# Performance work log

Measured on AMD Instinct MI355X. Metric: run time of the kernel, lower is better.

The kernel has to match this reference:

```python
import jax, jax.numpy as jnp
import numpy as np

N, Q, K, H, C = 32, 1, 2048, 16, 64
E = H * C  # 1024
N_ACT = 2


def setup_inputs() -> dict:
    key = jax.random.key(0)
    ks = jax.random.split(key, 8)
    q = jax.random.normal(ks[0], (N, Q, E), dtype=jnp.float32)
    k = jax.random.normal(ks[1], (N, K, H, C), dtype=jnp.float32)
    v = jax.random.normal(ks[2], (N, K, H, C), dtype=jnp.float32)
    m = jnp.ones((N, K), dtype=bool)
    s_in = 1.0 / np.sqrt(E)
    W_in = jax.random.uniform(ks[3], (N_ACT * E, E), jnp.float32, -s_in, s_in)
    b_in = jax.random.uniform(ks[4], (N_ACT * E,), jnp.float32, -s_in, s_in)
    W_out = jax.random.uniform(ks[5], (E, E), jnp.float32, -s_in, s_in)
    b_out = jax.random.uniform(ks[6], (E,), jnp.float32, -s_in, s_in)
    return {"q": q, "k": k, "v": v, "m": m, "W_in": W_in, "b_in": b_in,
            "W_out": W_out, "b_out": b_out}


def reference(q, k, v, m, W_in, b_in, W_out, b_out):
    norm = jnp.sqrt(jnp.asarray(C, q.dtype))
    # in_proj then split into per-branch queries: [N,Q,H,C] each
    qp = (q @ W_in.T + b_in).reshape(N, Q, H, N_ACT * C)
    q_smax, q_coda = qp[..., :C], qp[..., C:]
    mexp = m[:, None, :, None]  # [N,1,K,1]

    # branch 1: masked softmax over keys
    aff_s = jnp.einsum('nqhc,nkhc->nqkh', q_smax / norm, k)
    aff_s = jnp.where(mexp, aff_s, -jnp.inf)
    aff_s = jax.nn.softmax(aff_s, axis=-2)

    # branch 2: compositional de-attention (tanh affinity * sigmoid gate)
    aff_c = jnp.tanh(jnp.einsum('nqhc,nkhc->nqkh', q_coda / norm, k))
    gate = -jnp.abs(q_coda[:, :, None] - k[:, None]).sum(-1) / norm  # [N,Q,K,H]
    gate = 2.0 * jax.nn.sigmoid(gate) * mexp.astype(q.dtype)
    aff_c = aff_c * gate

    aff = (aff_s + aff_c) / N_ACT
    mix = jnp.einsum('nqkh,nkhc->nqhc', aff, v)  # [N,Q,H,C]
    return mix.reshape(N, Q, E) @ W_out.T + b_out
```

## Files before the change

kernel.cpp:

```cpp
#include <hip/hip_runtime.h>

#define NB 32
#define KK 2048
#define HH 16
#define CC 64
#define EE 1024
#define RIN 2048
#define HC 1024
#define CHUNK 32
#define NCH (KK / CHUNK)

__device__ __forceinline__ float dot4(const float4 a, const float4 b) {
    return fmaf(a.x, b.x, fmaf(a.y, b.y, fmaf(a.z, b.z, a.w * b.w)));
}

__device__ __forceinline__ float rcp_fast(float x) {
    return __builtin_amdgcn_rcpf(x);
}

__device__ __forceinline__ float tanh_fast(float x) {
    x = fminf(fmaxf(x, -15.0f), 15.0f);
    float t = __expf(2.0f * x);
    return (t - 1.0f) * rcp_fast(t + 1.0f);
}

__device__ __forceinline__ float gate_fn(float a) {
    return 2.0f * rcp_fast(1.0f + __expf(a));
}

__device__ __forceinline__ void gload_lds16(const float* g, float* l) {
    __builtin_amdgcn_global_load_lds(
        (const __attribute__((address_space(1))) void*)g,
        (__attribute__((address_space(3))) void*)l,
        16, 0, 2);
}

__global__ __launch_bounds__(256) void gemv_batched(
        const float* __restrict__ X,
        const float* __restrict__ W,
        const float* __restrict__ b,
        float* __restrict__ Y,
        int ystride) {
    const int tid  = threadIdx.x;
    const int lane = tid & 63;
    const int w    = tid >> 6;
    const int r    = blockIdx.x * 4 + w;
    const float* Wr = W + (size_t)r * EE;

    float acc[NB];
#pragma unroll
    for (int n = 0; n < NB; ++n) acc[n] = 0.0f;

#pragma unroll
    for (int ch = 0; ch < EE; ch += 256) {
        const float4 wv = *(const float4*)(Wr + ch + lane * 4);
#pragma unroll
        for (int n = 0; n < NB; ++n) {
            const float4 xv = *(const float4*)(X + n * EE + ch + lane * 4);
            acc[n] = fmaf(wv.x, xv.x, acc[n]);
            acc[n] = fmaf(wv.y, xv.y, acc[n]);
            acc[n] = fmaf(wv.z, xv.z, acc[n]);
            acc[n] = fmaf(wv.w, xv.w, acc[n]);
        }
    }
#pragma unroll
    for (int n = 0; n < NB; ++n) {
#pragma unroll
        for (int m = 32; m >= 1; m >>= 1)
            acc[n] += __shfl_xor(acc[n], m);
    }
    if (lane == 0) {
        const float bb = b[r];
#pragma unroll
        for (int n = 0; n < NB; ++n)
            Y[n * ystride + r] = acc[n] + bb;
    }
}

#define ABLK 512
__global__ __launch_bounds__(ABLK, 4) void attn_kernel(
        const float* __restrict__ Kp,
        const float* __restrict__ Vp,
        const float* __restrict__ qp,
        float* __restrict__ mix) {
    __shared__ float bufK[4][CHUNK][CC];
    __shared__ float bufV[4][CHUNK][CC];
    __shared__ float A_part[8][CC];
    __shared__ float C_part[8][CC];
    __shared__ float redm[8];
    __shared__ float reds[8];

    const int tid  = threadIdx.x;
    const int lane = tid & 63;
    const int w    = tid >> 6;
    const int rw   = lane >> 4;
    const int c16  = lane & 15;
    const int n    = blockIdx.x >> 4;
    const int h    = blockIdx.x & 15;

    const float* qrow = qp + n * RIN + h * (2 * CC) + c16 * 4;
    const float4 qs = *(const float4*)(qrow);
    const float4 qc = *(const float4*)(qrow + CC);

    const size_t base = (size_t)n * KK * HC + h * CC;
    const float* kb = Kp + base;
    const float* vb = Vp + base;

    const size_t g_lane_off = (size_t)(lane >> 4) * HC + (lane & 15) * 4;

#define STAGE(c, slot)                                                          \
    {                                                                           \
        const size_t ro_ = (size_t)((c) * CHUNK + w * 4) * HC + g_lane_off;     \
        gload_lds16(kb + ro_, &bufK[(slot)][w * 4][0]);                         \
        gload_lds16(vb + ro_, &bufV[(slot)][w * 4][0]);                         \
    }

#define WAITV(c)                                                                \
    {                                                                           \
        if ((c) <= NCH - 3)      asm volatile("s_waitcnt vmcnt(4)" ::: "memory"); \
        else if ((c) == NCH - 2) asm volatile("s_waitcnt vmcnt(2)" ::: "memory"); \
        else                     asm volatile("s_waitcnt vmcnt(0)" ::: "memory"); \
        __builtin_amdgcn_sched_barrier(0);                                      \
    }

#define BAR_LGKM()                                                              \
    {                                                                           \
        asm volatile("s_waitcnt lgkmcnt(0)" ::: "memory");                      \
        __builtin_amdgcn_s_barrier();                                           \
        __builtin_amdgcn_sched_barrier(0);                                      \
    }

#define COMP(c, slot)                                                           \
    {                                                                           \
        const int r_ = w * 4 + rw;                                              \
        const float4 kv = *(const float4*)&bufK[(slot)][r_][c16 * 4];           \
        const float4 vv = *(const float4*)&bufV[(slot)][r_][c16 * 4];           \
        float ds = dot4(qs, kv);                                                \
        float dc = dot4(qc, kv);                                                \
        float ga = fabsf(qc.x - kv.x) + fabsf(qc.y - kv.y)                      \
                 + fabsf(qc.z - kv.z) + fabsf(qc.w - kv.w);                     \
        ds += __shfl_xor(ds, 1); ds += __shfl_xor(ds, 2);                       \
        ds += __shfl_xor(ds, 4); ds += __shfl_xor(ds, 8);                       \
        dc += __shfl_xor(dc, 1); dc += __shfl_xor(dc, 2);                       \
        dc += __shfl_xor(dc, 4); dc += __shfl_xor(dc, 8);                       \
        ga += __shfl_xor(ga, 1); ga += __shfl_xor(ga, 2);                       \
        ga += __shfl_xor(ga, 4); ga += __shfl_xor(ga, 8);                       \
        const float s_   = ds * 0.125f;                                         \
        const float cval = tanh_fast(dc * 0.125f) * gate_fn(ga * 0.125f);       \
        const float mn = fmaxf(m_run, s_);                                      \
        const float f  = __expf(m_run - mn);                                    \
        const float e  = __expf(s_ - mn);                                       \
        m_run = mn;                                                             \
        S_run = fmaf(S_run, f, e);                                              \
        A.x = fmaf(A.x, f, e * vv.x); A.y = fmaf(A.y, f, e * vv.y);             \
        A.z = fmaf(A.z, f, e * vv.z); A.w = fmaf(A.w, f, e * vv.w);             \
        Cv.x = fmaf(cval, vv.x, Cv.x); Cv.y = fmaf(cval, vv.y, Cv.y);           \
        Cv.z = fmaf(cval, vv.z, Cv.z); Cv.w = fmaf(cval, vv.w, Cv.w);           \
    }

    float m_run = -1e30f, S_run = 0.0f;
    float4 A  = make_float4(0.f, 0.f, 0.f, 0.f);
    float4 Cv = make_float4(0.f, 0.f, 0.f, 0.f);

    STAGE(0, 0); STAGE(1, 1); STAGE(2, 2);
    for (int cc = 0; cc < NCH; cc += 4) {
        WAITV(cc + 0);
        STAGE(cc + 3, 3);
        COMP(cc + 0, 0);
        WAITV(cc + 1);
        if (cc + 4 < NCH) STAGE(cc + 4, 0);
        COMP(cc + 1, 1);
        WAITV(cc + 2);
        if (cc + 5 < NCH) STAGE(cc + 5, 1);
        COMP(cc + 2, 2);
        WAITV(cc + 3);
        if (cc + 6 < NCH) STAGE(cc + 6, 2);
        COMP(cc + 3, 3);
    }

    float mw = m_run;
    mw = fmaxf(mw, __shfl_xor(mw, 16));
    mw = fmaxf(mw, __shfl_xor(mw, 32));
    if (lane == 0) redm[w] = mw;
    BAR_LGKM();
    float M = redm[0];
#pragma unroll
    for (int ww = 1; ww < 8; ++ww) M = fmaxf(M, redm[ww]);

    const float f = __expf(m_run - M);
    S_run *= f;
    A.x *= f; A.y *= f; A.z *= f; A.w *= f;
#pragma unroll
    for (int m = 16; m <= 32; m <<= 1) {
        S_run += __shfl_xor(S_run, m);
        A.x += __shfl_xor(A.x, m); A.y += __shfl_xor(A.y, m);
        A.z += __shfl_xor(A.z, m); A.w += __shfl_xor(A.w, m);
        Cv.x += __shfl_xor(Cv.x, m); Cv.y += __shfl_xor(Cv.y, m);
        Cv.z += __shfl_xor(Cv.z, m); Cv.w += __shfl_xor(Cv.w, m);
    }
    if (lane < 16) {
        *(float4*)&A_part[w][c16 * 4] = A;
        *(float4*)&C_part[w][c16 * 4] = Cv;
    }
    if (lane == 0) reds[w] = S_run;
    BAR_LGKM();
    if (tid < CC) {
        float St = 0.0f;
#pragma unroll
        for (int ww = 0; ww < 8; ++ww) St += reds[ww];
        float a = 0.0f, c_ = 0.0f;
#pragma unroll
        for (int ww = 0; ww < 8; ++ww) {
            a  += A_part[ww][tid];
            c_ += C_part[ww][tid];
        }
        mix[n * EE + h * CC + tid] = a * (0.5f / St) + 0.5f * c_;
    }
#undef STAGE
#undef WAITV
#undef BAR_LGKM
#undef COMP
}

extern "C" void kernel_launch(void* const* d_in, const int* in_sizes, int n_in,
                              void* d_out, int out_size, void* d_ws, size_t ws_size,
                              hipStream_t stream) {
    const float* q     = (const float*)d_in[0];
    const float* k     = (const float*)d_in[1];
    const float* v     = (const float*)d_in[2];
    const float* W_in  = (const float*)d_in[4];
    const float* b_in  = (const float*)d_in[5];
    const float* W_out = (const float*)d_in[6];
    const float* b_out = (const float*)d_in[7];
    float* out = (float*)d_out;

    float* qp  = (float*)d_ws;
    float* mix = qp + NB * RIN;

    gemv_batched<<<RIN / 4, 256, 0, stream>>>(q, W_in, b_in, qp, RIN);
    attn_kernel<<<NB * HH, ABLK, 0, stream>>>(k, v, qp, mix);
    gemv_batched<<<EE / 4, 256, 0, stream>>>(mix, W_out, b_out, out, EE);
}
```

Measured before the change: 137.8 us.

## Split attention over key segments with head-pair blocks and a merge kernel

```diff
diff --git a/kernel.cpp b/kernel.cpp
--- a/kernel.cpp
+++ b/kernel.cpp
@@ -7,11 +7,15 @@
 #define EE 1024
 #define RIN 2048
 #define HC 1024
-#define CHUNK 32
-#define NCH (KK / CHUNK)
-
-__device__ __forceinline__ float dot4(const float4 a, const float4 b) {
-    return fmaf(a.x, b.x, fmaf(a.y, b.y, fmaf(a.z, b.z, a.w * b.w)));
+#define NSEG 4
+#define SROWS (KK / NSEG)
+#define CHUNK 16
+#define NCH (SROWS / CHUNK)
+
+typedef float f32x4 __attribute__((ext_vector_type(4)));
+
+__device__ __forceinline__ float dot4f(const f32x4 a, const f32x4 b) {
+    return fmaf(a[0], b[0], fmaf(a[1], b[1], fmaf(a[2], b[2], a[3] * b[3])));
 }
 
 __device__ __forceinline__ float rcp_fast(float x) {
@@ -77,48 +81,58 @@
     }
 }
 
-#define ABLK 512
-__global__ __launch_bounds__(ABLK, 4) void attn_kernel(
+__global__ __launch_bounds__(256, 4) void attn_kernel(
         const float* __restrict__ Kp,
         const float* __restrict__ Vp,
         const float* __restrict__ qp,
-        float* __restrict__ mix) {
-    __shared__ float bufK[4][CHUNK][CC];
-    __shared__ float bufV[4][CHUNK][CC];
-    __shared__ float A_part[8][CC];
-    __shared__ float C_part[8][CC];
-    __shared__ float redm[8];
-    __shared__ float reds[8];
+        float* __restrict__ pm,
+        float* __restrict__ pS,
+        float* __restrict__ pA,
+        float* __restrict__ pC) {
+    __shared__ float bufK[4][CHUNK][128];
+    __shared__ float bufV[4][CHUNK][128];
+    __shared__ float A_part[4][128];
+    __shared__ float C_part[4][128];
+    __shared__ float redm[4][2];
+    __shared__ float reds[4][2];
 
     const int tid  = threadIdx.x;
     const int lane = tid & 63;
     const int w    = tid >> 6;
     const int rw   = lane >> 4;
     const int c16  = lane & 15;
-    const int n    = blockIdx.x >> 4;
-    const int h    = blockIdx.x & 15;
-
-    const float* qrow = qp + n * RIN + h * (2 * CC) + c16 * 4;
-    const float4 qs = *(const float4*)(qrow);
-    const float4 qc = *(const float4*)(qrow + CC);
-
-    const size_t base = (size_t)n * KK * HC + h * CC;
-    const float* kb = Kp + base;
-    const float* vb = Vp + base;
-
-    const size_t g_lane_off = (size_t)(lane >> 4) * HC + (lane & 15) * 4;
+    const int hb   = c16 >> 3;
+    const int b    = blockIdx.x;
+    const int n    = b >> 5;
+    const int hp   = (b >> 2) & 7;
+    const int s    = b & 3;
+
+    const int qh = hp * 2 + hb;
+    const float* qrow = qp + n * RIN + qh * (2 * CC) + (c16 & 7) * 8;
+    const f32x4 qsa = *(const f32x4*)(qrow);
+    const f32x4 qsb = *(const f32x4*)(qrow + 4);
+    const f32x4 qca = *(const f32x4*)(qrow + CC);
+    const f32x4 qcb = *(const f32x4*)(qrow + CC + 4);
+
+    const size_t gbase = ((size_t)n * KK + s * SROWS) * HC + hp * 128;
+    const float* kb0 = Kp + gbase;
+    const float* vb0 = Vp + gbase;
+
+    const size_t g_lane_off = (size_t)(lane >> 5) * HC + (lane & 31) * 4;
 
 #define STAGE(c, slot)                                                          \
     {                                                                           \
         const size_t ro_ = (size_t)((c) * CHUNK + w * 4) * HC + g_lane_off;     \
-        gload_lds16(kb + ro_, &bufK[(slot)][w * 4][0]);                         \
-        gload_lds16(vb + ro_, &bufV[(slot)][w * 4][0]);                         \
+        gload_lds16(kb0 + ro_,                  &bufK[(slot)][w * 4][0]);       \
+        gload_lds16(kb0 + ro_ + 2 * (size_t)HC, &bufK[(slot)][w * 4 + 2][0]);   \
+        gload_lds16(vb0 + ro_,                  &bufV[(slot)][w * 4][0]);       \
+        gload_lds16(vb0 + ro_ + 2 * (size_t)HC, &bufV[(slot)][w * 4 + 2][0]);   \
     }
 
 #define WAITV(c)                                                                \
     {                                                                           \
-        if ((c) <= NCH - 3)      asm volatile("s_waitcnt vmcnt(4)" ::: "memory"); \
-        else if ((c) == NCH - 2) asm volatile("s_waitcnt vmcnt(2)" ::: "memory"); \
+        if ((c) <= NCH - 3)      asm volatile("s_waitcnt vmcnt(8)" ::: "memory"); \
+        else if ((c) == NCH - 2) asm volatile("s_waitcnt vmcnt(4)" ::: "memory"); \
         else                     asm volatile("s_waitcnt vmcnt(0)" ::: "memory"); \
         __builtin_amdgcn_sched_barrier(0);                                      \
     }
@@ -130,96 +144,121 @@
         __builtin_amdgcn_sched_barrier(0);                                      \
     }
 
-#define COMP(c, slot)                                                           \
+#define COMP(slot)                                                              \
     {                                                                           \
         const int r_ = w * 4 + rw;                                              \
-        const float4 kv = *(const float4*)&bufK[(slot)][r_][c16 * 4];           \
-        const float4 vv = *(const float4*)&bufV[(slot)][r_][c16 * 4];           \
-        float ds = dot4(qs, kv);                                                \
-        float dc = dot4(qc, kv);                                                \
-        float ga = fabsf(qc.x - kv.x) + fabsf(qc.y - kv.y)                      \
-                 + fabsf(qc.z - kv.z) + fabsf(qc.w - kv.w);                     \
-        ds += __shfl_xor(ds, 1); ds += __shfl_xor(ds, 2);                       \
-        ds += __shfl_xor(ds, 4); ds += __shfl_xor(ds, 8);                       \
-        dc += __shfl_xor(dc, 1); dc += __shfl_xor(dc, 2);                       \
-        dc += __shfl_xor(dc, 4); dc += __shfl_xor(dc, 8);                       \
-        ga += __shfl_xor(ga, 1); ga += __shfl_xor(ga, 2);                       \
-        ga += __shfl_xor(ga, 4); ga += __shfl_xor(ga, 8);                       \
+        const f32x4 k0 = *(const f32x4*)&bufK[(slot)][r_][c16 * 8];             \
+        const f32x4 k1 = *(const f32x4*)&bufK[(slot)][r_][c16 * 8 + 4];         \
+        const f32x4 v0 = *(const f32x4*)&bufV[(slot)][r_][c16 * 8];             \
+        const f32x4 v1 = *(const f32x4*)&bufV[(slot)][r_][c16 * 8 + 4];         \
+        float ds = dot4f(qsa, k0) + dot4f(qsb, k1);                             \
+        float dc = dot4f(qca, k0) + dot4f(qcb, k1);                             \
+        float ga = fabsf(qca[0] - k0[0]) + fabsf(qca[1] - k0[1])                \
+                 + fabsf(qca[2] - k0[2]) + fabsf(qca[3] - k0[3])                \
+                 + fabsf(qcb[0] - k1[0]) + fabsf(qcb[1] - k1[1])                \
+                 + fabsf(qcb[2] - k1[2]) + fabsf(qcb[3] - k1[3]);               \
+        ds += __shfl_xor(ds, 1); ds += __shfl_xor(ds, 2); ds += __shfl_xor(ds, 4); \
+        dc += __shfl_xor(dc, 1); dc += __shfl_xor(dc, 2); dc += __shfl_xor(dc, 4); \
+        ga += __shfl_xor(ga, 1); ga += __shfl_xor(ga, 2); ga += __shfl_xor(ga, 4); \
         const float s_   = ds * 0.125f;                                         \
         const float cval = tanh_fast(dc * 0.125f) * gate_fn(ga * 0.125f);       \
         const float mn = fmaxf(m_run, s_);                                      \
-        const float f  = __expf(m_run - mn);                                    \
+        const float fr = __expf(m_run - mn);                                    \
         const float e  = __expf(s_ - mn);                                       \
         m_run = mn;                                                             \
-        S_run = fmaf(S_run, f, e);                                              \
-        A.x = fmaf(A.x, f, e * vv.x); A.y = fmaf(A.y, f, e * vv.y);             \
-        A.z = fmaf(A.z, f, e * vv.z); A.w = fmaf(A.w, f, e * vv.w);             \
-        Cv.x = fmaf(cval, vv.x, Cv.x); Cv.y = fmaf(cval, vv.y, Cv.y);           \
-        Cv.z = fmaf(cval, vv.z, Cv.z); Cv.w = fmaf(cval, vv.w, Cv.w);           \
+        S_run = fmaf(S_run, fr, e);                                             \
+        A0 = A0 * fr + v0 * e;  A1 = A1 * fr + v1 * e;                          \
+        Cv0 = Cv0 + v0 * cval;  Cv1 = Cv1 + v1 * cval;                          \
     }
 
     float m_run = -1e30f, S_run = 0.0f;
-    float4 A  = make_float4(0.f, 0.f, 0.f, 0.f);
-    float4 Cv = make_float4(0.f, 0.f, 0.f, 0.f);
+    f32x4 A0 = {0.f, 0.f, 0.f, 0.f}, A1 = A0, Cv0 = A0, Cv1 = A0;
 
     STAGE(0, 0); STAGE(1, 1); STAGE(2, 2);
     for (int cc = 0; cc < NCH; cc += 4) {
         WAITV(cc + 0);
         STAGE(cc + 3, 3);
-        COMP(cc + 0, 0);
+        COMP(0);
         WAITV(cc + 1);
         if (cc + 4 < NCH) STAGE(cc + 4, 0);
-        COMP(cc + 1, 1);
+        COMP(1);
         WAITV(cc + 2);
         if (cc + 5 < NCH) STAGE(cc + 5, 1);
-        COMP(cc + 2, 2);
+        COMP(2);
         WAITV(cc + 3);
         if (cc + 6 < NCH) STAGE(cc + 6, 2);
-        COMP(cc + 3, 3);
-    }
-
-    float mw = m_run;
-    mw = fmaxf(mw, __shfl_xor(mw, 16));
+        COMP(3);
+    }
+
+    float mw = fmaxf(m_run, __shfl_xor(m_run, 16));
     mw = fmaxf(mw, __shfl_xor(mw, 32));
-    if (lane == 0) redm[w] = mw;
+    if (rw == 0 && (c16 & 7) == 0) redm[w][hb] = mw;
     BAR_LGKM();
-    float M = redm[0];
-#pragma unroll
-    for (int ww = 1; ww < 8; ++ww) M = fmaxf(M, redm[ww]);
-
-    const float f = __expf(m_run - M);
-    S_run *= f;
-    A.x *= f; A.y *= f; A.z *= f; A.w *= f;
+    const float M = fmaxf(fmaxf(redm[0][hb], redm[1][hb]),
+                          fmaxf(redm[2][hb], redm[3][hb]));
+
+    const float fr = __expf(m_run - M);
+    S_run *= fr;
+    A0 = A0 * fr; A1 = A1 * fr;
+    S_run += __shfl_xor(S_run, 16); S_run += __shfl_xor(S_run, 32);
 #pragma unroll
     for (int m = 16; m <= 32; m <<= 1) {
-        S_run += __shfl_xor(S_run, m);
-        A.x += __shfl_xor(A.x, m); A.y += __shfl_xor(A.y, m);
-        A.z += __shfl_xor(A.z, m); A.w += __shfl_xor(A.w, m);
-        Cv.x += __shfl_xor(Cv.x, m); Cv.y += __shfl_xor(Cv.y, m);
-        Cv.z += __shfl_xor(Cv.z, m); Cv.w += __shfl_xor(Cv.w, m);
-    }
-    if (lane < 16) {
-        *(float4*)&A_part[w][c16 * 4] = A;
-        *(float4*)&C_part[w][c16 * 4] = Cv;
-    }
-    if (lane == 0) reds[w] = S_run;
+        A0[0] += __shfl_xor(A0[0], m); A0[1] += __shfl_xor(A0[1], m);
+        A0[2] += __shfl_xor(A0[2], m); A0[3] += __shfl_xor(A0[3], m);
+        A1[0] += __shfl_xor(A1[0], m); A1[1] += __shfl_xor(A1[1], m);
+        A1[2] += __shfl_xor(A1[2], m); A1[3] += __shfl_xor(A1[3], m);
+        Cv0[0] += __shfl_xor(Cv0[0], m); Cv0[1] += __shfl_xor(Cv0[1], m);
+        Cv0[2] += __shfl_xor(Cv0[2], m); Cv0[3] += __shfl_xor(Cv0[3], m);
+        Cv1[0] += __shfl_xor(Cv1[0], m); Cv1[1] += __shfl_xor(Cv1[1], m);
+        Cv1[2] += __shfl_xor(Cv1[2], m); Cv1[3] += __shfl_xor(Cv1[3], m);
+    }
+    if (rw == 0) {
+        *(f32x4*)&A_part[w][c16 * 8]     = A0;
+        *(f32x4*)&A_part[w][c16 * 8 + 4] = A1;
+        *(f32x4*)&C_part[w][c16 * 8]     = Cv0;
+        *(f32x4*)&C_part[w][c16 * 8 + 4] = Cv1;
+        if ((c16 & 7) == 0) reds[w][hb] = S_run;
+    }
     BAR_LGKM();
-    if (tid < CC) {
-        float St = 0.0f;
-#pragma unroll
-        for (int ww = 0; ww < 8; ++ww) St += reds[ww];
-        float a = 0.0f, c_ = 0.0f;
-#pragma unroll
-        for (int ww = 0; ww < 8; ++ww) {
-            a  += A_part[ww][tid];
-            c_ += C_part[ww][tid];
-        }
-        mix[n * EE + h * CC + tid] = a * (0.5f / St) + 0.5f * c_;
+    if (tid < 128) {
+        const int hb2 = tid >> 6;
+        const int c   = tid & 63;
+        const int idx = (n * HH + hp * 2 + hb2) * NSEG + s;
+        const float M2 = fmaxf(fmaxf(redm[0][hb2], redm[1][hb2]),
+                               fmaxf(redm[2][hb2], redm[3][hb2]));
+        const float St = reds[0][hb2] + reds[1][hb2] + reds[2][hb2] + reds[3][hb2];
+        const float a  = A_part[0][tid] + A_part[1][tid] + A_part[2][tid] + A_part[3][tid];
+        const float cs = C_part[0][tid] + C_part[1][tid] + C_part[2][tid] + C_part[3][tid];
+        pA[(size_t)idx * CC + c] = a;
+        pC[(size_t)idx * CC + c] = cs;
+        if (c == 0) { pm[idx] = M2; pS[idx] = St; }
     }
 #undef STAGE
 #undef WAITV
 #undef BAR_LGKM
 #undef COMP
+}
+
+__global__ __launch_bounds__(256) void merge_kernel(
+        const float* __restrict__ pm, const float* __restrict__ pS,
+        const float* __restrict__ pA, const float* __restrict__ pC,
+        float* __restrict__ mix) {
+    const int f  = blockIdx.x * 256 + threadIdx.x;
+    const int c  = f & 63;
+    const int nh = f >> 6;
+    const int i0 = nh * NSEG;
+    float M = pm[i0];
+#pragma unroll
+    for (int s = 1; s < NSEG; ++s) M = fmaxf(M, pm[i0 + s]);
+    float S = 0.0f, a = 0.0f, cs = 0.0f;
+#pragma unroll
+    for (int s = 0; s < NSEG; ++s) {
+        const float e = __expf(pm[i0 + s] - M);
+        S  += pS[i0 + s] * e;
+        a  += pA[(size_t)(i0 + s) * CC + c] * e;
+        cs += pC[(size_t)(i0 + s) * CC + c];
+    }
+    mix[f] = a * (0.5f / S) + 0.5f * cs;
 }
 
 extern "C" void kernel_launch(void* const* d_in, const int* in_sizes, int n_in,
@@ -235,9 +274,14 @@
     float* out = (float*)d_out;
 
     float* qp  = (float*)d_ws;
-    float* mix = qp + NB * RIN;
-
-    gemv_batched<<<RIN / 4, 256, 0, stream>>>(q, W_in, b_in, qp, RIN);
-    attn_kernel<<<NB * HH, ABLK, 0, stream>>>(k, v, qp, mix);
-    gemv_batched<<<EE / 4, 256, 0, stream>>>(mix, W_out, b_out, out, EE);
-}
+    float* pm  = qp  + NB * RIN;
+    float* pS  = pm  + NB * HH * NSEG;
+    float* pA  = pS  + NB * HH * NSEG;
+    float* pC  = pA  + NB * HH * NSEG * CC;
+    float* mix = pC  + NB * HH * NSEG * CC;
+
+    gemv_batched<<<RIN / 4,          256, 0, stream>>>(q, W_in, b_in, qp, RIN);
+    attn_kernel <<<NB * 8 * NSEG,    256, 0, stream>>>(k, v, qp, pm, pS, pA, pC);
+    merge_kernel<<<NB * EE / 256,    256, 0, stream>>>(pm, pS, pA, pC, mix);
+    gemv_batched<<<EE / 4,           256, 0, stream>>>(mix, W_out, b_out, out, EE);
+}
```

After: 130.4 us, median of 2. 1.06x faster.
